# Performance work log

Hardware: AMD Instinct MI355X
Metric: run time of the kernel (lower is better)

Reference implementation:

```python
import jax, jax.numpy as jnp
import numpy as np
import math

D_MODEL = 1024
D_HIDDEN = 64
H = 16
B = 2
N = 2048


def softmax_one(x, axis=-1):
    # exp(x - max) / (1 + sum(exp(x - max))) -- matches the torch code exactly
    m = jnp.max(x, axis=axis, keepdims=True)
    e = jnp.exp(x - m)
    return e / (1.0 + jnp.sum(e, axis=axis, keepdims=True))


def setup_inputs() -> dict:
    key = jax.random.key(0)
    ks = jax.random.split(key, 8)
    queries = jax.random.normal(ks[0], (B, N, D_MODEL), dtype=jnp.float32)
    keys = jax.random.normal(ks[1], (B, N, D_MODEL), dtype=jnp.float32)
    values = jax.random.normal(ks[2], (B, N, D_MODEL), dtype=jnp.float32)
    std = 0.02
    Wq = std * jax.random.normal(ks[3], (H * D_HIDDEN, D_MODEL), dtype=jnp.float32)
    Wk = std * jax.random.normal(ks[4], (H * D_HIDDEN, D_MODEL), dtype=jnp.float32)
    Wv = std * jax.random.normal(ks[5], (H * D_HIDDEN, D_MODEL), dtype=jnp.float32)
    Wo = std * jax.random.normal(ks[6], (D_MODEL, H * D_HIDDEN), dtype=jnp.float32)
    bq = jnp.zeros((H * D_HIDDEN,), jnp.float32)
    bk = jnp.zeros((H * D_HIDDEN,), jnp.float32)
    bv = jnp.zeros((H * D_HIDDEN,), jnp.float32)
    bo = jnp.zeros((D_MODEL,), jnp.float32)
    return {"queries": queries, "keys": keys, "values": values,
            "Wq": Wq, "bq": bq, "Wk": Wk, "bk": bk,
            "Wv": Wv, "bv": bv, "Wo": Wo, "bo": bo}


def reference(queries, keys, values, Wq, bq, Wk, bk, Wv, bv, Wo, bo):
    b_s, nq, _ = queries.shape
    nk = keys.shape[1]
    # projections: (b, n, h*dh) -> (b, h, n, dh)
    q = (queries @ Wq.T + bq).reshape(b_s, nq, H, D_HIDDEN).transpose(0, 2, 1, 3)
    k = (keys @ Wk.T + bk).reshape(b_s, nk, H, D_HIDDEN).transpose(0, 2, 1, 3)
    v = (values @ Wv.T + bv).reshape(b_s, nk, H, D_HIDDEN).transpose(0, 2, 1, 3)
    scale = 1.0 / math.sqrt(D_HIDDEN)
    scores = jnp.einsum('bhqd,bhkd->bhqk', q, k) * scale  # (b, h, nq, nk)
    attn = softmax_one(scores, axis=-1)  # dropout disabled (eval)
    out = jnp.einsum('bhqk,bhkd->bhqd', attn, v)  # (b, h, nq, dh)
    out = out.transpose(0, 2, 1, 3).reshape(b_s, nq, H * D_HIDDEN)
    out = out @ Wo.T + bo
    present = jnp.stack((k, v))  # (2, b, h, nk, dh)
    return (out, present)
```

## Files before the change

### kernel.cpp

```cpp
#include <hip/hip_runtime.h>
#include <math.h>

#define D_MODEL 1024
#define DH 64
#define NH 16
#define BS 2
#define SEQ 2048
#define MTOT (BS*SEQ)

typedef _Float16 f16x8 __attribute__((ext_vector_type(8)));
typedef _Float16 f16x4 __attribute__((ext_vector_type(4)));
typedef float f32x4 __attribute__((ext_vector_type(4)));
typedef unsigned int u32;

__device__ __forceinline__ void load_lds16(const void* g, void* l) {
    __builtin_amdgcn_global_load_lds(
        (const __attribute__((address_space(1))) u32*)g,
        (__attribute__((address_space(3))) u32*)l, 16, 0, 0);
}

__global__ __launch_bounds__(256) void convert_all_kernel(
    const float* __restrict__ s0, const float* __restrict__ s1, const float* __restrict__ s2,
    const float* __restrict__ s3, const float* __restrict__ s4, const float* __restrict__ s5,
    const float* __restrict__ s6,
    _Float16* __restrict__ d0, _Float16* __restrict__ d1, _Float16* __restrict__ d2,
    _Float16* __restrict__ d3, _Float16* __restrict__ d4, _Float16* __restrict__ d5,
    _Float16* __restrict__ d6, int nX, int nW)
{
    int y = blockIdx.y;
    const float* s; _Float16* d; int n;
    switch (y) {
        case 0: s = s0; d = d0; n = nX; break;
        case 1: s = s1; d = d1; n = nX; break;
        case 2: s = s2; d = d2; n = nX; break;
        case 3: s = s3; d = d3; n = nW; break;
        case 4: s = s4; d = d4; n = nW; break;
        case 5: s = s5; d = d5; n = nW; break;
        default: s = s6; d = d6; n = nW; break;
    }
    int i = (blockIdx.x * 256 + threadIdx.x) * 8;
    if (i < n) {
        float4 a = *(const float4*)(s + i);
        float4 b = *(const float4*)(s + i + 4);
        f16x8 o;
        o[0] = (_Float16)a.x; o[1] = (_Float16)a.y; o[2] = (_Float16)a.z; o[3] = (_Float16)a.w;
        o[4] = (_Float16)b.x; o[5] = (_Float16)b.y; o[6] = (_Float16)b.z; o[7] = (_Float16)b.w;
        *(f16x8*)(d + i) = o;
    }
}

__global__ __launch_bounds__(256) void qkv_proj_kernel(
    const _Float16* __restrict__ Xq, const _Float16* __restrict__ Xk, const _Float16* __restrict__ Xv,
    const _Float16* __restrict__ Wq, const _Float16* __restrict__ Wk, const _Float16* __restrict__ Wv,
    const float* __restrict__ bq, const float* __restrict__ bk, const float* __restrict__ bv,
    _Float16* __restrict__ qh, _Float16* __restrict__ kh,
    float* __restrict__ outp)
{
    __shared__ __align__(16) _Float16 ldsA[2][128][64];
    __shared__ __align__(16) _Float16 ldsB[2][128][64];

    const int jb = blockIdx.x >> 5;
    const int ib = blockIdx.x & 31;
    const int id = jb >> 3;
    const int col0 = (jb & 7) << 7;
    const int row0 = ib << 7;

    const _Float16* X  = (id == 0) ? Xq : (id == 1) ? Xk : Xv;
    const _Float16* W  = (id == 0) ? Wq : (id == 1) ? Wk : Wv;
    const float* bias  = (id == 0) ? bq : (id == 1) ? bk : bv;

    const int tid = threadIdx.x;
    const int w = tid >> 6, lane = tid & 63;
    const int quad = lane >> 4, l16 = lane & 15;
    const int wm = (w >> 1) << 6, wn = (w & 1) << 6;

    const int r_loc = lane >> 3;
    const int sg = ((lane & 7) ^ r_loc) << 3;

    const f32x4 zero = {0.f, 0.f, 0.f, 0.f};
    f32x4 acc[4][4];
#pragma unroll
    for (int i = 0; i < 4; i++)
#pragma unroll
        for (int j = 0; j < 4; j++) acc[i][j] = zero;

#pragma unroll
    for (int i = 0; i < 4; i++) {
        int r = i * 32 + w * 8;
        load_lds16(X + (size_t)(row0 + r + r_loc) * D_MODEL + sg, &ldsA[0][r][0]);
        load_lds16(W + (size_t)(col0 + r + r_loc) * D_MODEL + sg, &ldsB[0][r][0]);
    }
    __syncthreads();

    for (int t = 0; t < D_MODEL / 64; t++) {
        const int cur = t & 1;

        if (t + 1 < D_MODEL / 64) {
            const int k1 = (t + 1) << 6;
#pragma unroll
            for (int i = 0; i < 4; i++) {
                int r = i * 32 + w * 8;
                load_lds16(X + (size_t)(row0 + r + r_loc) * D_MODEL + k1 + sg, &ldsA[cur ^ 1][r][0]);
                load_lds16(W + (size_t)(col0 + r + r_loc) * D_MODEL + k1 + sg, &ldsB[cur ^ 1][r][0]);
            }
        }

#pragma unroll
        for (int kk = 0; kk < 2; kk++) {
            f16x8 af[4], bfr[4];
#pragma unroll
            for (int mi = 0; mi < 4; mi++)
                af[mi]  = *(const f16x8*)&ldsA[cur][wm + mi*16 + l16][(((kk<<2) + quad) ^ (l16 & 7)) << 3];
#pragma unroll
            for (int ni = 0; ni < 4; ni++)
                bfr[ni] = *(const f16x8*)&ldsB[cur][wn + ni*16 + l16][(((kk<<2) + quad) ^ (l16 & 7)) << 3];
#pragma unroll
            for (int mi = 0; mi < 4; mi++)
#pragma unroll
                for (int ni = 0; ni < 4; ni++)
                    acc[mi][ni] = __builtin_amdgcn_mfma_f32_16x16x32_f16(af[mi], bfr[ni], acc[mi][ni], 0, 0, 0);
        }

        __syncthreads();
    }

    const size_t OUT0 = (size_t)MTOT * D_MODEL;
    const size_t PRES = (size_t)BS * NH * SEQ * DH;
#pragma unroll
    for (int ni = 0; ni < 4; ni++) {
        int gn = col0 + wn + ni * 16 + l16;
        float bias_v = bias[gn];
        int h = gn >> 6, d = gn & 63;
#pragma unroll
        for (int mi = 0; mi < 4; mi++) {
#pragma unroll
            for (int r = 0; r < 4; r++) {
                int gm = row0 + wm + mi * 16 + quad * 4 + r;
                float val = acc[mi][ni][r] + bias_v;
                int b = gm >> 11, n = gm & 2047;
                size_t bh = (size_t)(b * NH + h);
                size_t idx = (bh * SEQ + n) * DH + d;
                if (id == 0) {
                    qh[idx] = (_Float16)val;
                } else if (id == 1) {
                    outp[OUT0 + idx] = val;
                    kh[idx] = (_Float16)val;
                } else {
                    outp[OUT0 + PRES + idx] = val;
                }
            }
        }
    }
}

__global__ __launch_bounds__(256) void vtrans_kernel(
    const float* __restrict__ p1, _Float16* __restrict__ vt)
{
    const int bh = blockIdx.x >> 6, nt = blockIdx.x & 63;
    const int tid = threadIdx.x;
    const int d = tid & 63, n8 = tid >> 6;
    const int n0 = nt * 32 + n8 * 8;
    const float* src = p1 + ((size_t)bh * SEQ + n0) * DH + d;
    f16x8 o;
#pragma unroll
    for (int i = 0; i < 8; i++) o[i] = (_Float16)src[(size_t)i * DH];
    *(f16x8*)(vt + ((size_t)bh * DH + d) * SEQ + n0) = o;
}

__global__ __launch_bounds__(512) void attn_kernel(
    const _Float16* __restrict__ qh, const _Float16* __restrict__ kh,
    const _Float16* __restrict__ vt, _Float16* __restrict__ aout)
{
    __shared__ __align__(16) _Float16 Kt[2][64][76];
    __shared__ __align__(16) _Float16 Vt[2][64][76];

    const int bh = blockIdx.x & 31;
    const int qt = blockIdx.x >> 5;
    const int b = bh >> 4, h = bh & 15;
    const int tid = threadIdx.x;
    const int w = tid >> 6, lane = tid & 63;
    const int quad = lane >> 4, l16 = lane & 15;
    const int qr0 = qt * 128 + w * 16;

    const _Float16* Qb = qh + (size_t)bh * SEQ * DH;
    const _Float16* Kb = kh + (size_t)bh * SEQ * DH;
    const _Float16* Vb = vt + (size_t)bh * DH * SEQ;

    const float QSCALE = 0.125f * 1.44269504f;
    f16x8 aq[2];
#pragma unroll
    for (int ks = 0; ks < 2; ks++) {
        f16x8 t = *(const f16x8*)(Qb + (size_t)(qr0 + l16) * DH + ks * 32 + quad * 8);
#pragma unroll
        for (int j = 0; j < 8; j++) t[j] = (_Float16)((float)t[j] * QSCALE);
        aq[ks] = t;
    }

    const int sr = tid >> 3, sc = (tid & 7) << 3;

    *(f16x8*)&Kt[0][sr][sc] = *(const f16x8*)(Kb + (size_t)sr * DH + sc);
    *(f16x8*)&Vt[0][sr][sc] = *(const f16x8*)(Vb + (size_t)sr * SEQ + sc);
    __syncthreads();

    float m2 = -INFINITY, lsum = 0.f;
    const f32x4 zero = {0.f, 0.f, 0.f, 0.f};
    f32x4 accO[4];
#pragma unroll
    for (int db = 0; db < 4; db++) accO[db] = zero;

    for (int t = 0; t < SEQ / 64; t++) {
        const int cur = t & 1;
        const int kc = t * 64;

        f16x8 kr, vr;
        if (t + 1 < SEQ / 64) {
            kr = *(const f16x8*)(Kb + (size_t)(kc + 64 + sr) * DH + sc);
            vr = *(const f16x8*)(Vb + (size_t)sr * SEQ + kc + 64 + sc);
        }

        f32x4 sT[4];
#pragma unroll
        for (int nb = 0; nb < 4; nb++) sT[nb] = zero;
#pragma unroll
        for (int ks = 0; ks < 2; ks++)
#pragma unroll
            for (int nb = 0; nb < 4; nb++) {
                f16x8 kf = *(const f16x8*)&Kt[cur][nb*16 + l16][ks*32 + quad*8];
                sT[nb] = __builtin_amdgcn_mfma_f32_16x16x32_f16(kf, aq[ks], sT[nb], 0, 0, 0);
            }

        f16x4 pf[4];
#pragma unroll
        for (int nb = 0; nb < 4; nb++)
#pragma unroll
            for (int r = 0; r < 4; r++) {
                float s = sT[nb][r];
                m2 = fmaxf(m2, s);
                float e = __builtin_amdgcn_exp2f(s);
                lsum += e;
                pf[nb][r] = (_Float16)e;
            }

#pragma unroll
        for (int db = 0; db < 4; db++)
#pragma unroll
            for (int nb = 0; nb < 4; nb++) {
                f16x4 vf = *(const f16x4*)&Vt[cur][db*16 + l16][nb*16 + quad*4];
                accO[db] = __builtin_amdgcn_mfma_f32_16x16x16f16(vf, pf[nb], accO[db], 0, 0, 0);
            }

        if (t + 1 < SEQ / 64) {
            *(f16x8*)&Kt[cur ^ 1][sr][sc] = kr;
            *(f16x8*)&Vt[cur ^ 1][sr][sc] = vr;
        }
        __syncthreads();
    }

    m2 = fmaxf(m2, __shfl_xor(m2, 16));
    m2 = fmaxf(m2, __shfl_xor(m2, 32));
    lsum += __shfl_xor(lsum, 16);
    lsum += __shfl_xor(lsum, 32);

    const float inv = 1.f / (__builtin_amdgcn_exp2f(m2) + lsum);
    const int q = qr0 + l16;
    _Float16* orow = aout + ((size_t)b * SEQ + q) * D_MODEL + h * DH + quad * 4;
#pragma unroll
    for (int db = 0; db < 4; db++) {
        f16x4 o;
#pragma unroll
        for (int r = 0; r < 4; r++) o[r] = (_Float16)(accO[db][r] * inv);
        *(f16x4*)(orow + db * 16) = o;
    }
}

__global__ __launch_bounds__(256) void out_proj_kernel(
    const _Float16* __restrict__ aout, const _Float16* __restrict__ Wo,
    const float* __restrict__ bo, float* __restrict__ outp)
{
    __shared__ __align__(16) _Float16 ldsA[2][64][64];
    __shared__ __align__(16) _Float16 ldsB[2][128][64];

    const int jb = blockIdx.x >> 6;
    const int ib = blockIdx.x & 63;
    const int col0 = jb << 7, row0 = ib << 6;
    const int tid = threadIdx.x;
    const int w = tid >> 6, lane = tid & 63;
    const int quad = lane >> 4, l16 = lane & 15;
    const int wm = (w >> 1) << 5, wn = (w & 1) << 6;

    const int r_loc = lane >> 3;
    const int sg = ((lane & 7) ^ r_loc) << 3;

    const f32x4 zero = {0.f, 0.f, 0.f, 0.f};
    f32x4 acc[2][4];
#pragma unroll
    for (int i = 0; i < 2; i++)
#pragma unroll
        for (int j = 0; j < 4; j++) acc[i][j] = zero;

#pragma unroll
    for (int i = 0; i < 2; i++) {
        int r = i * 32 + w * 8;
        load_lds16(aout + (size_t)(row0 + r + r_loc) * D_MODEL + sg, &ldsA[0][r][0]);
    }
#pragma unroll
    for (int i = 0; i < 4; i++) {
        int r = i * 32 + w * 8;
        load_lds16(Wo + (size_t)(col0 + r + r_loc) * D_MODEL + sg, &ldsB[0][r][0]);
    }
    __syncthreads();

    for (int t = 0; t < D_MODEL / 64; t++) {
        const int cur = t & 1;

        if (t + 1 < D_MODEL / 64) {
            const int k1 = (t + 1) << 6;
#pragma unroll
            for (int i = 0; i < 2; i++) {
                int r = i * 32 + w * 8;
                load_lds16(aout + (size_t)(row0 + r + r_loc) * D_MODEL + k1 + sg, &ldsA[cur ^ 1][r][0]);
            }
#pragma unroll
            for (int i = 0; i < 4; i++) {
                int r = i * 32 + w * 8;
                load_lds16(Wo + (size_t)(col0 + r + r_loc) * D_MODEL + k1 + sg, &ldsB[cur ^ 1][r][0]);
            }
        }

#pragma unroll
        for (int kk = 0; kk < 2; kk++) {
            f16x8 af[2], bfr[4];
#pragma unroll
            for (int mi = 0; mi < 2; mi++)
                af[mi]  = *(const f16x8*)&ldsA[cur][wm + mi*16 + l16][(((kk<<2) + quad) ^ (l16 & 7)) << 3];
#pragma unroll
            for (int ni = 0; ni < 4; ni++)
                bfr[ni] = *(const f16x8*)&ldsB[cur][wn + ni*16 + l16][(((kk<<2) + quad) ^ (l16 & 7)) << 3];
#pragma unroll
            for (int mi = 0; mi < 2; mi++)
#pragma unroll
                for (int ni = 0; ni < 4; ni++)
                    acc[mi][ni] = __builtin_amdgcn_mfma_f32_16x16x32_f16(af[mi], bfr[ni], acc[mi][ni], 0, 0, 0);
        }

        __syncthreads();
    }

#pragma unroll
    for (int ni = 0; ni < 4; ni++) {
        int gn = col0 + wn + ni * 16 + l16;
        float bias_v = bo[gn];
#pragma unroll
        for (int mi = 0; mi < 2; mi++)
#pragma unroll
            for (int r = 0; r < 4; r++) {
                int gm = row0 + wm + mi * 16 + quad * 4 + r;
                outp[(size_t)gm * D_MODEL + gn] = acc[mi][ni][r] + bias_v;
            }
    }
}

extern "C" void kernel_launch(void* const* d_in, const int* in_sizes, int n_in,
                              void* d_out, int out_size, void* d_ws, size_t ws_size,
                              hipStream_t stream)
{
    const float* queries = (const float*)d_in[0];
    const float* keys    = (const float*)d_in[1];
    const float* values  = (const float*)d_in[2];
    const float* Wq = (const float*)d_in[3];
    const float* bq = (const float*)d_in[4];
    const float* Wk = (const float*)d_in[5];
    const float* bk = (const float*)d_in[6];
    const float* Wv = (const float*)d_in[7];
    const float* bv = (const float*)d_in[8];
    const float* Wo = (const float*)d_in[9];
    const float* bo = (const float*)d_in[10];
    float* outp = (float*)d_out;

    const size_t NELT = (size_t)BS * NH * SEQ * DH;
    const size_t XN   = (size_t)MTOT * D_MODEL;
    const size_t WN   = (size_t)D_MODEL * D_MODEL;
    _Float16* qh   = (_Float16*)d_ws;
    _Float16* kh   = qh + NELT;
    _Float16* vt   = kh + NELT;
    _Float16* aout = vt + NELT;
    _Float16* Xfq  = aout + NELT;
    _Float16* Xfk  = Xfq + XN;
    _Float16* Xfv  = Xfk + XN;
    _Float16* Wfq  = Xfv + XN;
    _Float16* Wfk  = Wfq + WN;
    _Float16* Wfv  = Wfk + WN;
    _Float16* Wfo  = Wfv + WN;

    const size_t OUT0 = (size_t)MTOT * D_MODEL;
    const size_t PRES = NELT;
    const float* present1 = outp + OUT0 + PRES;

    convert_all_kernel<<<dim3((int)(XN/2048), 7), dim3(256), 0, stream>>>(
        queries, keys, values, Wq, Wk, Wv, Wo,
        Xfq, Xfk, Xfv, Wfq, Wfk, Wfv, Wfo, (int)XN, (int)WN);

    qkv_proj_kernel<<<dim3(768), dim3(256), 0, stream>>>(
        Xfq, Xfk, Xfv, Wfq, Wfk, Wfv, bq, bk, bv, qh, kh, outp);
    vtrans_kernel<<<dim3(2048), dim3(256), 0, stream>>>(present1, vt);
    attn_kernel<<<dim3(512), dim3(512), 0, stream>>>(qh, kh, vt, aout);
    out_proj_kernel<<<dim3(512), dim3(256), 0, stream>>>(aout, Wfo, bo, outp);
}
```

Baseline: 245.7 us.

## Fuse V transpose into QKV projection epilogue and use vmcnt-based barriers

The separate vtrans kernel is removed. The QKV projection epilogue now writes the transposed fp16 V directly as f16x4 vectors along the sequence dimension, which saves a launch and a re-read of the fp32 V present tensor. Both GEMM loops also replace the trailing __syncthreads with explicit s_waitcnt vmcnt counts plus raw s_barrier, so the LDS prefetch of the next tile can stay in flight while the current tile is computed. The hand-written vmcnt counts depend on the exact number of outstanding loads and could break correctness if the compiler reorders them.

```diff
diff --git a/kernel.cpp b/kernel.cpp
--- a/kernel.cpp
+++ b/kernel.cpp
@@ -53,7 +53,7 @@
     const _Float16* __restrict__ Xq, const _Float16* __restrict__ Xk, const _Float16* __restrict__ Xv,
     const _Float16* __restrict__ Wq, const _Float16* __restrict__ Wk, const _Float16* __restrict__ Wv,
     const float* __restrict__ bq, const float* __restrict__ bk, const float* __restrict__ bv,
-    _Float16* __restrict__ qh, _Float16* __restrict__ kh,
+    _Float16* __restrict__ qh, _Float16* __restrict__ kh, _Float16* __restrict__ vt,
     float* __restrict__ outp)
 {
     __shared__ __align__(16) _Float16 ldsA[2][128][64];
@@ -90,10 +90,11 @@
         load_lds16(X + (size_t)(row0 + r + r_loc) * D_MODEL + sg, &ldsA[0][r][0]);
         load_lds16(W + (size_t)(col0 + r + r_loc) * D_MODEL + sg, &ldsB[0][r][0]);
     }
-    __syncthreads();
 
     for (int t = 0; t < D_MODEL / 64; t++) {
         const int cur = t & 1;
+
+        __builtin_amdgcn_s_barrier();
 
         if (t + 1 < D_MODEL / 64) {
             const int k1 = (t + 1) << 6;
@@ -103,7 +104,12 @@
                 load_lds16(X + (size_t)(row0 + r + r_loc) * D_MODEL + k1 + sg, &ldsA[cur ^ 1][r][0]);
                 load_lds16(W + (size_t)(col0 + r + r_loc) * D_MODEL + k1 + sg, &ldsB[cur ^ 1][r][0]);
             }
-        }
+            asm volatile("s_waitcnt vmcnt(8)" ::: "memory");
+        } else {
+            asm volatile("s_waitcnt vmcnt(0)" ::: "memory");
+        }
+
+        __builtin_amdgcn_s_barrier();
 
 #pragma unroll
         for (int kk = 0; kk < 2; kk++) {
@@ -120,8 +126,6 @@
                 for (int ni = 0; ni < 4; ni++)
                     acc[mi][ni] = __builtin_amdgcn_mfma_f32_16x16x32_f16(af[mi], bfr[ni], acc[mi][ni], 0, 0, 0);
         }
-
-        __syncthreads();
     }
 
     const size_t OUT0 = (size_t)MTOT * D_MODEL;
@@ -133,38 +137,35 @@
         int h = gn >> 6, d = gn & 63;
 #pragma unroll
         for (int mi = 0; mi < 4; mi++) {
-#pragma unroll
-            for (int r = 0; r < 4; r++) {
-                int gm = row0 + wm + mi * 16 + quad * 4 + r;
-                float val = acc[mi][ni][r] + bias_v;
-                int b = gm >> 11, n = gm & 2047;
-                size_t bh = (size_t)(b * NH + h);
-                size_t idx = (bh * SEQ + n) * DH + d;
-                if (id == 0) {
-                    qh[idx] = (_Float16)val;
-                } else if (id == 1) {
+            int gm0 = row0 + wm + mi * 16 + quad * 4;
+            int b = gm0 >> 11, n0 = gm0 & 2047;
+            size_t bh = (size_t)(b * NH + h);
+            if (id == 0) {
+#pragma unroll
+                for (int r = 0; r < 4; r++) {
+                    float val = acc[mi][ni][r] + bias_v;
+                    qh[(bh * SEQ + n0 + r) * DH + d] = (_Float16)val;
+                }
+            } else if (id == 1) {
+#pragma unroll
+                for (int r = 0; r < 4; r++) {
+                    float val = acc[mi][ni][r] + bias_v;
+                    size_t idx = (bh * SEQ + n0 + r) * DH + d;
                     outp[OUT0 + idx] = val;
                     kh[idx] = (_Float16)val;
-                } else {
-                    outp[OUT0 + PRES + idx] = val;
                 }
-            }
-        }
-    }
-}
-
-__global__ __launch_bounds__(256) void vtrans_kernel(
-    const float* __restrict__ p1, _Float16* __restrict__ vt)
-{
-    const int bh = blockIdx.x >> 6, nt = blockIdx.x & 63;
-    const int tid = threadIdx.x;
-    const int d = tid & 63, n8 = tid >> 6;
-    const int n0 = nt * 32 + n8 * 8;
-    const float* src = p1 + ((size_t)bh * SEQ + n0) * DH + d;
-    f16x8 o;
-#pragma unroll
-    for (int i = 0; i < 8; i++) o[i] = (_Float16)src[(size_t)i * DH];
-    *(f16x8*)(vt + ((size_t)bh * DH + d) * SEQ + n0) = o;
+            } else {
+                f16x4 o;
+#pragma unroll
+                for (int r = 0; r < 4; r++) {
+                    float val = acc[mi][ni][r] + bias_v;
+                    outp[OUT0 + PRES + (bh * SEQ + n0 + r) * DH + d] = val;
+                    o[r] = (_Float16)val;
+                }
+                *(f16x4*)(vt + (bh * DH + d) * SEQ + n0) = o;
+            }
+        }
+    }
 }
 
 __global__ __launch_bounds__(512) void attn_kernel(
@@ -308,10 +309,11 @@
         int r = i * 32 + w * 8;
         load_lds16(Wo + (size_t)(col0 + r + r_loc) * D_MODEL + sg, &ldsB[0][r][0]);
     }
-    __syncthreads();
 
     for (int t = 0; t < D_MODEL / 64; t++) {
         const int cur = t & 1;
+
+        __builtin_amdgcn_s_barrier();
 
         if (t + 1 < D_MODEL / 64) {
             const int k1 = (t + 1) << 6;
@@ -325,7 +327,12 @@
                 int r = i * 32 + w * 8;
                 load_lds16(Wo + (size_t)(col0 + r + r_loc) * D_MODEL + k1 + sg, &ldsB[cur ^ 1][r][0]);
             }
-        }
+            asm volatile("s_waitcnt vmcnt(6)" ::: "memory");
+        } else {
+            asm volatile("s_waitcnt vmcnt(0)" ::: "memory");
+        }
+
+        __builtin_amdgcn_s_barrier();
 
 #pragma unroll
         for (int kk = 0; kk < 2; kk++) {
@@ -342,8 +349,6 @@
                 for (int ni = 0; ni < 4; ni++)
                     acc[mi][ni] = __builtin_amdgcn_mfma_f32_16x16x32_f16(af[mi], bfr[ni], acc[mi][ni], 0, 0, 0);
         }
-
-        __syncthreads();
     }
 
 #pragma unroll
@@ -392,17 +397,12 @@
     _Float16* Wfv  = Wfk + WN;
     _Float16* Wfo  = Wfv + WN;
 
-    const size_t OUT0 = (size_t)MTOT * D_MODEL;
-    const size_t PRES = NELT;
-    const float* present1 = outp + OUT0 + PRES;
-
     convert_all_kernel<<<dim3((int)(XN/2048), 7), dim3(256), 0, stream>>>(
         queries, keys, values, Wq, Wk, Wv, Wo,
         Xfq, Xfk, Xfv, Wfq, Wfk, Wfv, Wfo, (int)XN, (int)WN);
 
     qkv_proj_kernel<<<dim3(768), dim3(256), 0, stream>>>(
-        Xfq, Xfk, Xfv, Wfq, Wfk, Wfv, bq, bk, bv, qh, kh, outp);
-    vtrans_kernel<<<dim3(2048), dim3(256), 0, stream>>>(present1, vt);
+        Xfq, Xfk, Xfv, Wfq, Wfk, Wfv, bq, bk, bv, qh, kh, vt, outp);
     attn_kernel<<<dim3(512), dim3(512), 0, stream>>>(qh, kh, vt, aout);
     out_proj_kernel<<<dim3(512), dim3(256), 0, stream>>>(aout, Wfo, bo, outp);
 }
```

Measured after the change: 233.7 us. 4.9% less time.

## Use partial vmcnt waits in GEMMs and vectorize V loads with permuted transpose

Applied to the files above, without the earlier changes.

The projection and output GEMMs swap the full __syncthreads after each k-step for raw s_barriers plus s_waitcnt vmcnt(N). Each step now waits only for the previous tile's global-to-LDS loads while the next tile's loads stay in flight, so the prefetch overlaps the MFMAs better. The V transpose kernel writes positions in a permuted order within each 64-key block. That lets the attention PV step read V as two 16-byte LDS loads per row instead of four 8-byte loads, while keeping the PV product unchanged. The code relies on exact vmcnt counts and barrier placement, which is fragile if the compiler reorders or adds memory ops.

```diff
diff --git a/kernel.cpp b/kernel.cpp
--- a/kernel.cpp
+++ b/kernel.cpp
@@ -90,10 +90,11 @@
         load_lds16(X + (size_t)(row0 + r + r_loc) * D_MODEL + sg, &ldsA[0][r][0]);
         load_lds16(W + (size_t)(col0 + r + r_loc) * D_MODEL + sg, &ldsB[0][r][0]);
     }
-    __syncthreads();
 
     for (int t = 0; t < D_MODEL / 64; t++) {
         const int cur = t & 1;
+
+        __builtin_amdgcn_s_barrier();
 
         if (t + 1 < D_MODEL / 64) {
             const int k1 = (t + 1) << 6;
@@ -103,7 +104,12 @@
                 load_lds16(X + (size_t)(row0 + r + r_loc) * D_MODEL + k1 + sg, &ldsA[cur ^ 1][r][0]);
                 load_lds16(W + (size_t)(col0 + r + r_loc) * D_MODEL + k1 + sg, &ldsB[cur ^ 1][r][0]);
             }
-        }
+            asm volatile("s_waitcnt vmcnt(8)" ::: "memory");
+        } else {
+            asm volatile("s_waitcnt vmcnt(0)" ::: "memory");
+        }
+
+        __builtin_amdgcn_s_barrier();
 
 #pragma unroll
         for (int kk = 0; kk < 2; kk++) {
@@ -120,8 +126,6 @@
                 for (int ni = 0; ni < 4; ni++)
                     acc[mi][ni] = __builtin_amdgcn_mfma_f32_16x16x32_f16(af[mi], bfr[ni], acc[mi][ni], 0, 0, 0);
         }
-
-        __syncthreads();
     }
 
     const size_t OUT0 = (size_t)MTOT * D_MODEL;
@@ -160,10 +164,16 @@
     const int tid = threadIdx.x;
     const int d = tid & 63, n8 = tid >> 6;
     const int n0 = nt * 32 + n8 * 8;
-    const float* src = p1 + ((size_t)bh * SEQ + n0) * DH + d;
+    const int tb = n0 & ~63;
+    const int p0 = n0 & 63;
+    const float* src = p1 + ((size_t)bh * SEQ + tb) * DH + d;
     f16x8 o;
 #pragma unroll
-    for (int i = 0; i < 8; i++) o[i] = (_Float16)src[(size_t)i * DH];
+    for (int i = 0; i < 8; i++) {
+        int p = p0 + i;
+        int k = ((p & 0x30) >> 2) | ((p & 0x0C) << 2) | (p & 3);
+        o[i] = (_Float16)src[(size_t)k * DH];
+    }
     *(f16x8*)(vt + ((size_t)bh * DH + d) * SEQ + n0) = o;
 }
 
@@ -242,12 +252,18 @@
             }
 
 #pragma unroll
-        for (int db = 0; db < 4; db++)
-#pragma unroll
-            for (int nb = 0; nb < 4; nb++) {
-                f16x4 vf = *(const f16x4*)&Vt[cur][db*16 + l16][nb*16 + quad*4];
-                accO[db] = __builtin_amdgcn_mfma_f32_16x16x16f16(vf, pf[nb], accO[db], 0, 0, 0);
-            }
+        for (int db = 0; db < 4; db++) {
+            f16x8 v01 = *(const f16x8*)&Vt[cur][db*16 + l16][quad*16];
+            f16x8 v23 = *(const f16x8*)&Vt[cur][db*16 + l16][quad*16 + 8];
+            f16x4 vf0 = __builtin_shufflevector(v01, v01, 0, 1, 2, 3);
+            f16x4 vf1 = __builtin_shufflevector(v01, v01, 4, 5, 6, 7);
+            f16x4 vf2 = __builtin_shufflevector(v23, v23, 0, 1, 2, 3);
+            f16x4 vf3 = __builtin_shufflevector(v23, v23, 4, 5, 6, 7);
+            accO[db] = __builtin_amdgcn_mfma_f32_16x16x16f16(vf0, pf[0], accO[db], 0, 0, 0);
+            accO[db] = __builtin_amdgcn_mfma_f32_16x16x16f16(vf1, pf[1], accO[db], 0, 0, 0);
+            accO[db] = __builtin_amdgcn_mfma_f32_16x16x16f16(vf2, pf[2], accO[db], 0, 0, 0);
+            accO[db] = __builtin_amdgcn_mfma_f32_16x16x16f16(vf3, pf[3], accO[db], 0, 0, 0);
+        }
 
         if (t + 1 < SEQ / 64) {
             *(f16x8*)&Kt[cur ^ 1][sr][sc] = kr;
@@ -308,10 +324,11 @@
         int r = i * 32 + w * 8;
         load_lds16(Wo + (size_t)(col0 + r + r_loc) * D_MODEL + sg, &ldsB[0][r][0]);
     }
-    __syncthreads();
 
     for (int t = 0; t < D_MODEL / 64; t++) {
         const int cur = t & 1;
+
+        __builtin_amdgcn_s_barrier();
 
         if (t + 1 < D_MODEL / 64) {
             const int k1 = (t + 1) << 6;
@@ -325,7 +342,12 @@
                 int r = i * 32 + w * 8;
                 load_lds16(Wo + (size_t)(col0 + r + r_loc) * D_MODEL + k1 + sg, &ldsB[cur ^ 1][r][0]);
             }
-        }
+            asm volatile("s_waitcnt vmcnt(6)" ::: "memory");
+        } else {
+            asm volatile("s_waitcnt vmcnt(0)" ::: "memory");
+        }
+
+        __builtin_amdgcn_s_barrier();
 
 #pragma unroll
         for (int kk = 0; kk < 2; kk++) {
@@ -342,8 +364,6 @@
                 for (int ni = 0; ni < 4; ni++)
                     acc[mi][ni] = __builtin_amdgcn_mfma_f32_16x16x32_f16(af[mi], bfr[ni], acc[mi][ni], 0, 0, 0);
         }
-
-        __syncthreads();
     }
 
 #pragma unroll
```

Result: faster. 239.6 us (-2.5%).
